# Kernel tuning notes

Measured on AMD Instinct MI355X. Metric: run time of the kernel, lower is better.

Reference implementation:

```python
import jax, jax.numpy as jnp
import numpy as np

CAPACITY = 0.7
TEMP = 0.5          # initial_temp, never annealed (global_step=None path)
LB_WEIGHT = 0.005
Z_WEIGHT = 5e-06
EPS = 1e-10


def setup_inputs() -> dict:
    key = jax.random.key(0)
    k1, k2, k3 = jax.random.split(key, 3)
    B, S, H = 4, 8192, 2048
    return {
        "hidden_states": jax.random.normal(k1, (B, S, H), dtype=jnp.float32),
        "active_mask": jnp.ones((B, S), dtype=bool),
        "u": jax.random.uniform(k2, (B, S), dtype=jnp.float32),
        # router: nn.Linear(H, 1), weight ~ N(0, 0.02), bias = 0
        "w": jax.random.normal(k3, (H,), dtype=jnp.float32) * 0.02,
        "b": jnp.zeros((), dtype=jnp.float32),
    }


def reference(hidden_states, active_mask, u, w, b):
    B, S = active_mask.shape
    N = B * S
    # mask is all-True by construction -> num_active = N, k static
    num_active = N
    k = max(1, min(int(CAPACITY * num_active), num_active))

    # scores = router(hidden).squeeze(-1)  -> [B,S]
    scores = jnp.einsum("bsh,h->bs", hidden_states, w) + b
    scores = jnp.where(active_mask, scores, -jnp.inf)

    # gumbel noise from uniform u (matches torch.rand_like path)
    gumbel = -jnp.log(-jnp.log(u + EPS) + EPS)
    noisy = ((scores + gumbel) / TEMP).reshape(-1)  # [N]

    _, idx = jax.lax.top_k(noisy, k)
    ffn_mask = jnp.zeros((N,), dtype=bool).at[idx].set(True)
    ffn_mask = ffn_mask.reshape(B, S) & active_mask

    # aux losses (masked reductions over active tokens)
    maskf = active_mask.astype(jnp.float32)
    na = maskf.sum()
    safe_scores = jnp.where(active_mask, scores, 0.0)
    f = ffn_mask.astype(jnp.float32).sum() / na
    p = (jax.nn.sigmoid(safe_scores) * maskf).sum() / na
    lb_loss = (f - CAPACITY) ** 2 + (p - CAPACITY) ** 2
    z_loss = (safe_scores ** 2 * maskf).sum() / na
    aux_loss = LB_WEIGHT * lb_loss + Z_WEIGHT * z_loss

    return ffn_mask, aux_loss
```

## Files before the change

kernel.cpp:

```cpp
#include <hip/hip_runtime.h>
#include <math.h>

#define NTOK 32768
#define HDIM 2048
#define K_SEL 22937
#define EPS_F 1e-10f
#define SBLK 1024

__global__ __launch_bounds__(256) void score_kernel(
    const float* __restrict__ hidden,
    const float* __restrict__ u,
    const float* __restrict__ w,
    const float* __restrict__ b,
    unsigned int* __restrict__ keys,
    float* __restrict__ pp,
    float* __restrict__ zz)
{
    const int wave = threadIdx.x >> 6;
    const int lane = threadIdx.x & 63;
    const int row0 = blockIdx.x * 32 + wave * 8;

    const float4* __restrict__ w4 = (const float4*)w;
    float4 wr[8];
    #pragma unroll
    for (int j = 0; j < 8; ++j) wr[j] = w4[j * 64 + lane];

    const float4* __restrict__ rowp = (const float4*)(hidden + (size_t)row0 * HDIM);

    float sums[8];
    float4 buf[2][8];
    #pragma unroll
    for (int j = 0; j < 8; ++j) buf[0][j] = rowp[j * 64 + lane];

    #pragma unroll
    for (int r = 0; r < 8; ++r) {
        const int cur = r & 1, nxt = cur ^ 1;
        if (r < 7) {
            #pragma unroll
            for (int j = 0; j < 8; ++j)
                buf[nxt][j] = rowp[(r + 1) * 512 + j * 64 + lane];
        }
        float s = 0.0f;
        #pragma unroll
        for (int j = 0; j < 8; ++j) {
            const float4 hv = buf[cur][j];
            s += hv.x * wr[j].x + hv.y * wr[j].y + hv.z * wr[j].z + hv.w * wr[j].w;
        }
        sums[r] = s;
    }

    #pragma unroll
    for (int off = 32; off > 0; off >>= 1) {
        #pragma unroll
        for (int r = 0; r < 8; ++r)
            sums[r] += __shfl_down(sums[r], off, 64);
    }

    __shared__ float red_p[4], red_z[4];
    if (lane == 0) {
        const float bias = b[0];
        float p_acc = 0.0f, z_acc = 0.0f;
        #pragma unroll
        for (int r = 0; r < 8; ++r) {
            const float score = sums[r] + bias;
            const float uu = u[row0 + r];
            const float g = -logf(-logf(uu + EPS_F) + EPS_F);
            const float noisy = (score + g) * 2.0f;
            const unsigned int bits = __float_as_uint(noisy);
            keys[row0 + r] = (bits & 0x80000000u) ? ~bits : (bits | 0x80000000u);
            p_acc += 1.0f / (1.0f + expf(-score));
            z_acc += score * score;
        }
        red_p[wave] = p_acc;
        red_z[wave] = z_acc;
    }
    __syncthreads();
    if (threadIdx.x == 0) {
        pp[blockIdx.x] = red_p[0] + red_p[1] + red_p[2] + red_p[3];
        zz[blockIdx.x] = red_z[0] + red_z[1] + red_z[2] + red_z[3];
    }
}

__global__ __launch_bounds__(1024) void select_kernel(
    const unsigned int* __restrict__ keys,
    const float* __restrict__ pp,
    const float* __restrict__ zz,
    float* __restrict__ out)
{
    __shared__ unsigned int sbuf[8448];
    __shared__ unsigned int wcnt[16];
    __shared__ float wredp[16], wredz[16];
    __shared__ unsigned int wtot[16], woff[16];

    const int t = threadIdx.x;
    const int lane = t & 63;
    const int wid = t >> 6;

    unsigned int myk[32];
    for (int p = 0; p < 4; ++p) {
        #pragma unroll
        for (int q = 0; q < 2; ++q) {
            const int v4idx = t + 1024 * q;
            const int e = 4 * v4idx;
            const uint4 kv = ((const uint4*)(keys + 8192 * p))[v4idx];
            *((uint4*)&sbuf[e + (e >> 5)]) = kv;
        }
        __syncthreads();
        const int c = t - 256 * p;
        if (c >= 0 && c < 256) {
            #pragma unroll
            for (int j = 0; j < 8; ++j) {
                const uint4 kv = *((const uint4*)&sbuf[33 * c + 4 * j]);
                myk[4 * j + 0] = kv.x;
                myk[4 * j + 1] = kv.y;
                myk[4 * j + 2] = kv.z;
                myk[4 * j + 3] = kv.w;
            }
        }
        __syncthreads();
    }

    unsigned int tau = 0u;
    for (int bit = 31; bit >= 0; --bit) {
        const unsigned int cand = tau | (1u << bit);
        unsigned int c = 0u;
        #pragma unroll
        for (int j = 0; j < 32; ++j) c += (myk[j] >= cand) ? 1u : 0u;
        #pragma unroll
        for (int off = 32; off > 0; off >>= 1) c += __shfl_down(c, off, 64);
        if (lane == 0) wcnt[wid] = c;
        __syncthreads();
        unsigned int tot = 0u;
        #pragma unroll
        for (int i = 0; i < 16; ++i) tot += wcnt[i];
        if (tot >= (unsigned int)K_SEL) tau = cand;
        __syncthreads();
    }

    unsigned int cgt = 0u;
    #pragma unroll
    for (int j = 0; j < 32; ++j) cgt += (myk[j] > tau) ? 1u : 0u;
    unsigned int cg = cgt;
    #pragma unroll
    for (int off = 32; off > 0; off >>= 1) cg += __shfl_down(cg, off, 64);
    if (lane == 0) wcnt[wid] = cg;
    __syncthreads();
    unsigned int tot_gt = 0u;
    #pragma unroll
    for (int i = 0; i < 16; ++i) tot_gt += wcnt[i];
    const unsigned int needed = (unsigned int)K_SEL - tot_gt;

    unsigned int ceq = 0u;
    #pragma unroll
    for (int j = 0; j < 32; ++j) ceq += (myk[j] == tau) ? 1u : 0u;
    unsigned int v = ceq;
    #pragma unroll
    for (int off = 1; off < 64; off <<= 1) {
        const unsigned int n = __shfl_up(v, off, 64);
        if (lane >= off) v += n;
    }
    __syncthreads();
    if (lane == 63) wtot[wid] = v;
    __syncthreads();
    if (t == 0) {
        unsigned int run = 0u;
        for (int i = 0; i < 16; ++i) { woff[i] = run; run += wtot[i]; }
    }
    __syncthreads();
    unsigned int rank = woff[wid] + (v - ceq);

    for (int p = 0; p < 4; ++p) {
        const int c = t - 256 * p;
        if (c >= 0 && c < 256) {
            #pragma unroll
            for (int j = 0; j < 32; ++j) {
                const unsigned int kk = myk[j];
                float val;
                if (kk > tau) {
                    val = 1.0f;
                } else if (kk == tau) {
                    val = (rank < needed) ? 1.0f : 0.0f;
                    rank++;
                } else {
                    val = 0.0f;
                }
                const int e = 32 * c + j;
                ((float*)sbuf)[e + (e >> 5)] = val;
            }
        }
        __syncthreads();
        #pragma unroll
        for (int q = 0; q < 2; ++q) {
            const int v4idx = t + 1024 * q;
            const int e = 4 * v4idx;
            const float4 fv = *((const float4*)&((float*)sbuf)[e + (e >> 5)]);
            ((float4*)(out + 8192 * p))[v4idx] = fv;
        }
        __syncthreads();
    }

    float lp = pp[t], lz = zz[t];
    #pragma unroll
    for (int off = 32; off > 0; off >>= 1) {
        lp += __shfl_down(lp, off, 64);
        lz += __shfl_down(lz, off, 64);
    }
    if (lane == 0) { wredp[wid] = lp; wredz[wid] = lz; }
    __syncthreads();
    if (t == 0) {
        float sp = 0.0f, sz = 0.0f;
        for (int i = 0; i < 16; ++i) { sp += wredp[i]; sz += wredz[i]; }
        const float na = (float)NTOK;
        const float f = (float)K_SEL / na;
        const float p = sp / na;
        const float z = sz / na;
        const float d1 = f - 0.7f;
        const float d2 = p - 0.7f;
        out[NTOK] = 0.005f * (d1 * d1 + d2 * d2) + 5e-6f * z;
    }
}

extern "C" void kernel_launch(void* const* d_in, const int* in_sizes, int n_in,
                              void* d_out, int out_size, void* d_ws, size_t ws_size,
                              hipStream_t stream) {
    const float* hidden = (const float*)d_in[0];
    const float* u = (const float*)d_in[2];
    const float* w = (const float*)d_in[3];
    const float* b = (const float*)d_in[4];
    float* out = (float*)d_out;

    const size_t KEYS_BYTES = (size_t)NTOK * sizeof(unsigned int);
    const size_t PART_BYTES = (size_t)SBLK * sizeof(float);

    unsigned int* keys;
    float *pp, *zz;
    if (ws_size >= KEYS_BYTES + 2 * PART_BYTES) {
        keys = (unsigned int*)d_ws;
        pp = (float*)((char*)d_ws + KEYS_BYTES);
        zz = pp + SBLK;
    } else {
        keys = (unsigned int*)d_out;
        pp = (float*)d_ws;
        zz = pp + SBLK;
    }

    score_kernel<<<SBLK, 256, 0, stream>>>(hidden, u, w, b, keys, pp, zz);
    select_kernel<<<1, 1024, 0, stream>>>(keys, pp, zz, out);
}
```

Before: 406.5 us.

## Build radix histogram during scoring to shortcut top-k threshold search

The score kernel now atomically builds a 16-bit-prefix histogram of the sortable keys. A single-block kernel uses that histogram to find the top bits of the threshold, then needs only the remaining 16 bit-steps of block-wide counting, and resolves ties by searching for a cutoff index instead of a serial rank scan. A separate multi-block kernel writes the mask. This removes many serialized block reductions and the shared-memory transposes from the single-block select kernel, at the cost of global atomics in the score kernel plus two extra launches (zeroing and masking).

```diff
diff --git a/kernel.cpp b/kernel.cpp
--- a/kernel.cpp
+++ b/kernel.cpp
@@ -6,6 +6,11 @@
 #define K_SEL 22937
 #define EPS_F 1e-10f
 #define SBLK 1024
+
+__global__ void zero_kernel(uint4* __restrict__ h4)
+{
+    h4[blockIdx.x * 256 + threadIdx.x] = make_uint4(0u, 0u, 0u, 0u);
+}
 
 __global__ __launch_bounds__(256) void score_kernel(
     const float* __restrict__ hidden,
@@ -14,7 +19,9 @@
     const float* __restrict__ b,
     unsigned int* __restrict__ keys,
     float* __restrict__ pp,
-    float* __restrict__ zz)
+    float* __restrict__ zz,
+    unsigned int* __restrict__ hist,
+    int shift)
 {
     const int wave = threadIdx.x >> 6;
     const int lane = threadIdx.x & 63;
@@ -67,7 +74,9 @@
             const float g = -logf(-logf(uu + EPS_F) + EPS_F);
             const float noisy = (score + g) * 2.0f;
             const unsigned int bits = __float_as_uint(noisy);
-            keys[row0 + r] = (bits & 0x80000000u) ? ~bits : (bits | 0x80000000u);
+            const unsigned int k = (bits & 0x80000000u) ? ~bits : (bits | 0x80000000u);
+            keys[row0 + r] = k;
+            atomicAdd(&hist[k >> shift], 1u);
             p_acc += 1.0f / (1.0f + expf(-score));
             z_acc += score * score;
         }
@@ -81,123 +90,125 @@
     }
 }
 
-__global__ __launch_bounds__(1024) void select_kernel(
+__global__ __launch_bounds__(1024) void tau_kernel(
     const unsigned int* __restrict__ keys,
+    const unsigned int* __restrict__ hist,
     const float* __restrict__ pp,
     const float* __restrict__ zz,
-    float* __restrict__ out)
-{
-    __shared__ unsigned int sbuf[8448];
+    unsigned int* __restrict__ meta,
+    float* __restrict__ out,
+    int shift)
+{
     __shared__ unsigned int wcnt[16];
+    __shared__ int sB;
     __shared__ float wredp[16], wredz[16];
-    __shared__ unsigned int wtot[16], woff[16];
 
     const int t = threadIdx.x;
     const int lane = t & 63;
     const int wid = t >> 6;
-
+    const int bins = 1 << (32 - shift);
+    const int g = bins >> 10;
+
+    unsigned int s = 0;
+    if ((g & 3) == 0) {
+        const uint4* h4 = (const uint4*)hist;
+        const int gq = g >> 2;
+        for (int i = 0; i < gq; ++i) {
+            const uint4 v = h4[t * gq + i];
+            s += v.x + v.y + v.z + v.w;
+        }
+    } else {
+        for (int i = 0; i < g; ++i) s += hist[t * g + i];
+    }
+    unsigned int suf = s;
+    #pragma unroll
+    for (int off = 1; off < 64; off <<= 1) {
+        const unsigned int n = __shfl_down(suf, off, 64);
+        if (lane + off < 64) suf += n;
+    }
+    if (lane == 0) wcnt[wid] = suf;
+    __syncthreads();
+    unsigned int hi = 0;
+    for (int i = wid + 1; i < 16; ++i) hi += wcnt[i];
+    const unsigned int SufT = suf + hi;
+    if (SufT >= (unsigned int)K_SEL && SufT - s < (unsigned int)K_SEL) {
+        unsigned int run = SufT - s;
+        for (int bb = g - 1; bb >= 0; --bb) {
+            run += hist[t * g + bb];
+            if (run >= (unsigned int)K_SEL) { sB = t * g + bb; break; }
+        }
+    }
+    __syncthreads();
+    unsigned int tau = ((unsigned int)sB) << shift;
+
+    uint4 k4[8];
+    const uint4* kk4 = (const uint4*)keys;
+    #pragma unroll
+    for (int j = 0; j < 8; ++j) k4[j] = kk4[1024 * j + t];
     unsigned int myk[32];
-    for (int p = 0; p < 4; ++p) {
-        #pragma unroll
-        for (int q = 0; q < 2; ++q) {
-            const int v4idx = t + 1024 * q;
-            const int e = 4 * v4idx;
-            const uint4 kv = ((const uint4*)(keys + 8192 * p))[v4idx];
-            *((uint4*)&sbuf[e + (e >> 5)]) = kv;
-        }
-        __syncthreads();
-        const int c = t - 256 * p;
-        if (c >= 0 && c < 256) {
-            #pragma unroll
-            for (int j = 0; j < 8; ++j) {
-                const uint4 kv = *((const uint4*)&sbuf[33 * c + 4 * j]);
-                myk[4 * j + 0] = kv.x;
-                myk[4 * j + 1] = kv.y;
-                myk[4 * j + 2] = kv.z;
-                myk[4 * j + 3] = kv.w;
-            }
-        }
-        __syncthreads();
-    }
-
-    unsigned int tau = 0u;
-    for (int bit = 31; bit >= 0; --bit) {
-        const unsigned int cand = tau | (1u << bit);
-        unsigned int c = 0u;
-        #pragma unroll
-        for (int j = 0; j < 32; ++j) c += (myk[j] >= cand) ? 1u : 0u;
+    #pragma unroll
+    for (int j = 0; j < 8; ++j) {
+        myk[4 * j + 0] = k4[j].x;
+        myk[4 * j + 1] = k4[j].y;
+        myk[4 * j + 2] = k4[j].z;
+        myk[4 * j + 3] = k4[j].w;
+    }
+
+    auto blocksum = [&](unsigned int c) -> unsigned int {
         #pragma unroll
         for (int off = 32; off > 0; off >>= 1) c += __shfl_down(c, off, 64);
         if (lane == 0) wcnt[wid] = c;
         __syncthreads();
-        unsigned int tot = 0u;
+        unsigned int tot = 0;
         #pragma unroll
         for (int i = 0; i < 16; ++i) tot += wcnt[i];
-        if (tot >= (unsigned int)K_SEL) tau = cand;
         __syncthreads();
-    }
-
-    unsigned int cgt = 0u;
-    #pragma unroll
-    for (int j = 0; j < 32; ++j) cgt += (myk[j] > tau) ? 1u : 0u;
-    unsigned int cg = cgt;
-    #pragma unroll
-    for (int off = 32; off > 0; off >>= 1) cg += __shfl_down(cg, off, 64);
-    if (lane == 0) wcnt[wid] = cg;
-    __syncthreads();
-    unsigned int tot_gt = 0u;
-    #pragma unroll
-    for (int i = 0; i < 16; ++i) tot_gt += wcnt[i];
+        return tot;
+    };
+
+    for (int bit = shift - 1; bit >= 0; --bit) {
+        const unsigned int cand = tau | (1u << bit);
+        unsigned int c = 0;
+        #pragma unroll
+        for (int m = 0; m < 32; ++m) c += (myk[m] >= cand) ? 1u : 0u;
+        if (blocksum(c) >= (unsigned int)K_SEL) tau = cand;
+    }
+
+    unsigned int cgt = 0, ceq = 0;
+    #pragma unroll
+    for (int m = 0; m < 32; ++m) {
+        cgt += (myk[m] > tau) ? 1u : 0u;
+        ceq += (myk[m] == tau) ? 1u : 0u;
+    }
+    const unsigned int totp = blocksum((cgt << 16) | ceq);
+    const unsigned int tot_gt = totp >> 16;
+    const unsigned int tot_eq = totp & 0xFFFFu;
     const unsigned int needed = (unsigned int)K_SEL - tot_gt;
 
-    unsigned int ceq = 0u;
-    #pragma unroll
-    for (int j = 0; j < 32; ++j) ceq += (myk[j] == tau) ? 1u : 0u;
-    unsigned int v = ceq;
-    #pragma unroll
-    for (int off = 1; off < 64; off <<= 1) {
-        const unsigned int n = __shfl_up(v, off, 64);
-        if (lane >= off) v += n;
-    }
-    __syncthreads();
-    if (lane == 63) wtot[wid] = v;
-    __syncthreads();
-    if (t == 0) {
-        unsigned int run = 0u;
-        for (int i = 0; i < 16; ++i) { woff[i] = run; run += wtot[i]; }
-    }
-    __syncthreads();
-    unsigned int rank = woff[wid] + (v - ceq);
-
-    for (int p = 0; p < 4; ++p) {
-        const int c = t - 256 * p;
-        if (c >= 0 && c < 256) {
+    unsigned int X = NTOK - 1;
+    if (needed < tot_eq) {
+        auto cntle = [&](unsigned int cand) -> unsigned int {
+            unsigned int c = 0;
             #pragma unroll
-            for (int j = 0; j < 32; ++j) {
-                const unsigned int kk = myk[j];
-                float val;
-                if (kk > tau) {
-                    val = 1.0f;
-                } else if (kk == tau) {
-                    val = (rank < needed) ? 1.0f : 0.0f;
-                    rank++;
-                } else {
-                    val = 0.0f;
-                }
-                const int e = 32 * c + j;
-                ((float*)sbuf)[e + (e >> 5)] = val;
+            for (int m = 0; m < 32; ++m) {
+                const unsigned int idx = 4096u * (m >> 2) + 4u * t + (m & 3);
+                c += (myk[m] == tau && idx <= cand) ? 1u : 0u;
             }
-        }
-        __syncthreads();
-        #pragma unroll
-        for (int q = 0; q < 2; ++q) {
-            const int v4idx = t + 1024 * q;
-            const int e = 4 * v4idx;
-            const float4 fv = *((const float4*)&((float*)sbuf)[e + (e >> 5)]);
-            ((float4*)(out + 8192 * p))[v4idx] = fv;
-        }
-        __syncthreads();
-    }
+            return blocksum(c);
+        };
+        if (cntle(0) >= needed) {
+            X = 0;
+        } else {
+            unsigned int Y = 0;
+            for (int bit = 14; bit >= 0; --bit) {
+                const unsigned int cand = Y | (1u << bit);
+                if (cntle(cand) < needed) Y = cand;
+            }
+            X = Y + 1;
+        }
+    }
+
+    if (t == 0) { meta[0] = tau; meta[1] = X; }
 
     float lp = pp[t], lz = zz[t];
     #pragma unroll
@@ -220,6 +231,24 @@
     }
 }
 
+__global__ __launch_bounds__(128) void mask_kernel(
+    const unsigned int* __restrict__ keys,
+    const unsigned int* __restrict__ meta,
+    float* __restrict__ out)
+{
+    const unsigned int tau = meta[0];
+    const unsigned int X = meta[1];
+    const int i = blockIdx.x * 128 + threadIdx.x;
+    const uint4 kv = ((const uint4*)keys)[i];
+    const unsigned int e = 4u * (unsigned int)i;
+    float4 o;
+    o.x = (kv.x > tau || (kv.x == tau && e     <= X)) ? 1.0f : 0.0f;
+    o.y = (kv.y > tau || (kv.y == tau && e + 1 <= X)) ? 1.0f : 0.0f;
+    o.z = (kv.z > tau || (kv.z == tau && e + 2 <= X)) ? 1.0f : 0.0f;
+    o.w = (kv.w > tau || (kv.w == tau && e + 3 <= X)) ? 1.0f : 0.0f;
+    ((float4*)out)[i] = o;
+}
+
 extern "C" void kernel_launch(void* const* d_in, const int* in_sizes, int n_in,
                               void* d_out, int out_size, void* d_ws, size_t ws_size,
                               hipStream_t stream) {
@@ -229,21 +258,41 @@
     const float* b = (const float*)d_in[4];
     float* out = (float*)d_out;
 
-    const size_t KEYS_BYTES = (size_t)NTOK * sizeof(unsigned int);
-    const size_t PART_BYTES = (size_t)SBLK * sizeof(float);
-
-    unsigned int* keys;
+    const size_t KEYS_B = (size_t)NTOK * sizeof(unsigned int);
+    const size_t PART_B = (size_t)SBLK * sizeof(float);
+    const size_t META_B = 256;
+    const size_t HIST16 = ((size_t)1 << 16) * sizeof(unsigned int);
+
+    int bits = 16;
+    char* wsp = (char*)d_ws;
+    unsigned int *keys, *hist, *meta;
     float *pp, *zz;
-    if (ws_size >= KEYS_BYTES + 2 * PART_BYTES) {
-        keys = (unsigned int*)d_ws;
-        pp = (float*)((char*)d_ws + KEYS_BYTES);
+
+    if (ws_size >= KEYS_B + 2 * PART_B + HIST16 + META_B) {
+        keys = (unsigned int*)wsp;
+        pp = (float*)(wsp + KEYS_B);
         zz = pp + SBLK;
+        hist = (unsigned int*)(wsp + KEYS_B + 2 * PART_B);
+        meta = hist + (1 << 16);
+    } else if (ws_size >= 2 * PART_B + HIST16 + META_B) {
+        keys = (unsigned int*)d_out;
+        pp = (float*)wsp;
+        zz = pp + SBLK;
+        hist = (unsigned int*)(wsp + 2 * PART_B);
+        meta = hist + (1 << 16);
     } else {
+        bits = 10;
         keys = (unsigned int*)d_out;
-        pp = (float*)d_ws;
+        pp = (float*)wsp;
         zz = pp + SBLK;
-    }
-
-    score_kernel<<<SBLK, 256, 0, stream>>>(hidden, u, w, b, keys, pp, zz);
-    select_kernel<<<1, 1024, 0, stream>>>(keys, pp, zz, out);
-}
+        hist = (unsigned int*)(wsp + 2 * PART_B);
+        meta = hist + (1 << 10);
+    }
+    const int shift = 32 - bits;
+    const int zblocks = (1 << bits) / 1024;
+
+    zero_kernel<<<zblocks, 256, 0, stream>>>((uint4*)hist);
+    score_kernel<<<SBLK, 256, 0, stream>>>(hidden, u, w, b, keys, pp, zz, hist, shift);
+    tau_kernel<<<1, 1024, 0, stream>>>(keys, hist, pp, zz, meta, out, shift);
+    mask_kernel<<<64, 128, 0, stream>>>(keys, meta, out);
+}
```

Measured after the change: 407.5 us. About the same (+0.2%).
